# Kernel tuning notes

Hardware: AMD Instinct MI355X
Metric: run time of the kernel (lower is better)

The kernel has to match this reference:

```python
import jax, jax.numpy as jnp
import numpy as np

NUM_HEADS = 16


def setup_inputs() -> dict:
    key = jax.random.key(0)
    k1, k2, k3, k4 = jax.random.split(key, 4)
    B, S, D = 2, 2048, 1024
    x = jax.random.normal(k1, (B, S, D), dtype=jnp.float32)
    W_qkv = jax.random.normal(k2, (D, 3 * D), dtype=jnp.float32) * (1.0 / np.sqrt(D))
    b_qkv = jax.random.normal(k3, (3 * D,), dtype=jnp.float32) * 0.02
    W_out = jax.random.normal(k4, (D, D), dtype=jnp.float32) * (1.0 / np.sqrt(D))
    return {"x": x, "W_qkv": W_qkv, "b_qkv": b_qkv, "W_out": W_out}


def reference(x, W_qkv, b_qkv, W_out):
    B, S, D = x.shape
    H = NUM_HEADS
    Hd = D // H
    scale = 1.0 / np.sqrt(Hd)

    qkv = x @ W_qkv + b_qkv                      # [B, S, 3D]
    q, k, v = jnp.split(qkv, 3, axis=-1)
    # [B, H, S, Hd]
    q = q.reshape(B, S, H, Hd).transpose(0, 2, 1, 3)
    k = k.reshape(B, S, H, Hd).transpose(0, 2, 1, 3)
    v = v.reshape(B, S, H, Hd).transpose(0, 2, 1, 3)

    scores = jnp.einsum('bhqd,bhkd->bhqk', q, k) * scale  # [B, H, S, S]
    causal = jnp.triu(jnp.full((S, S), -jnp.inf, dtype=scores.dtype), k=1)
    scores = scores + causal
    attn = jax.nn.softmax(scores.astype(jnp.float32), axis=-1).astype(q.dtype)

    ctx = jnp.einsum('bhqk,bhkd->bhqd', attn, v)           # [B, H, S, Hd]
    ctx = ctx.transpose(0, 2, 1, 3).reshape(B, S, D)
    return ctx @ W_out
```

## Files before the change

kernel.cpp:

```cpp
#include <hip/hip_runtime.h>
#include <hip/hip_bf16.h>

typedef __bf16 bf16x8 __attribute__((ext_vector_type(8)));
typedef float f32x4 __attribute__((ext_vector_type(4)));

typedef __attribute__((address_space(1))) void gv_t;
typedef __attribute__((address_space(3))) void lv_t;

__device__ __forceinline__ unsigned short f2bf(float f) {
    unsigned int u = __float_as_uint(f);
    unsigned int r = (u + 0x7fffu + ((u >> 16) & 1u)) >> 16;
    return (unsigned short)r;
}

__device__ __forceinline__ unsigned int cvt_pk_bf16(float a, float b) {
    unsigned int r;
    asm("v_cvt_pk_bf16_f32 %0, %1, %2" : "=v"(r) : "v"(a), "v"(b));
    return r;
}

__global__ __launch_bounds__(1024) void preprocess(const float* __restrict__ x,
                                                   const float* __restrict__ Wqkv,
                                                   const float* __restrict__ Wout,
                                                   unsigned short* __restrict__ x_bf,
                                                   unsigned short* __restrict__ wqkvT,
                                                   unsigned short* __restrict__ woutT) {
    const int bid = blockIdx.x, t = threadIdx.x;
    if (bid < 1024) {
        int i = bid * 1024 + t;
        float4 v = reinterpret_cast<const float4*>(x)[i];
        ushort4 o;
        o.x = f2bf(v.x); o.y = f2bf(v.y); o.z = f2bf(v.z); o.w = f2bf(v.w);
        reinterpret_cast<ushort4*>(x_bf)[i] = o;
        return;
    }
    __shared__ float tile[32][33];
    const int tx = t & 31, ty = t >> 5;
    const float* in;
    unsigned short* out;
    int K, N, n0, k0;
    if (bid < 4096) {
        int e = bid - 1024;
        in = Wqkv; out = wqkvT; K = 1024; N = 3072;
        n0 = (e % 96) * 32; k0 = (e / 96) * 32;
    } else {
        int e = bid - 4096;
        in = Wout; out = woutT; K = 1024; N = 1024;
        n0 = (e % 32) * 32; k0 = (e / 32) * 32;
    }
    tile[ty][tx] = in[(size_t)(k0 + ty) * N + (n0 + tx)];
    __syncthreads();
    out[(size_t)(n0 + ty) * K + (k0 + tx)] = f2bf(tile[tx][ty]);
}

template <bool BIAS, bool OUT_BF16, bool QSCALE>
__global__ __launch_bounds__(256) void gemm_bt(const unsigned short* __restrict__ A,
                                               const unsigned short* __restrict__ Bt,
                                               const float* __restrict__ bias,
                                               void* __restrict__ Cv,
                                               int M, int N, int K) {
    __shared__ alignas(16) unsigned short As[128 * 32];
    __shared__ alignas(16) unsigned short Bs[128 * 32];

    const int t = threadIdx.x;
    const int lane = t & 63;
    const int wid = t >> 6;
    const int wr = wid >> 1, wc = wid & 1;
    const int nwg = gridDim.x * gridDim.y;
    const int lin = blockIdx.y * gridDim.x + blockIdx.x;
    const int cpx = nwg >> 3;
    const int swz = (lin & 7) * cpx + (lin >> 3);
    const int m0 = (swz / gridDim.x) * 128, n0 = (swz % gridDim.x) * 128;

    f32x4 acc[4][4] = {};

    for (int k0 = 0; k0 < K; k0 += 32) {
#pragma unroll
        for (int i = 0; i < 2; ++i) {
            int c = i * 256 + t;
            int row = c >> 2;
            int col = (c & 3) * 8;
            const unsigned short* ga = A + (size_t)(m0 + row) * K + k0 + col;
            const unsigned short* gb = Bt + (size_t)(n0 + row) * K + k0 + col;
            __builtin_amdgcn_global_load_lds((gv_t*)ga, (lv_t*)(As + c * 8), 16, 0, 0);
            __builtin_amdgcn_global_load_lds((gv_t*)gb, (lv_t*)(Bs + c * 8), 16, 0, 0);
        }
        __syncthreads();

        bf16x8 af[4], bfr[4];
#pragma unroll
        for (int i = 0; i < 4; ++i)
            af[i] = *reinterpret_cast<const bf16x8*>(As + (wr * 64 + i * 16 + (lane & 15)) * 32 + (lane >> 4) * 8);
#pragma unroll
        for (int j = 0; j < 4; ++j)
            bfr[j] = *reinterpret_cast<const bf16x8*>(Bs + (wc * 64 + j * 16 + (lane & 15)) * 32 + (lane >> 4) * 8);
#pragma unroll
        for (int i = 0; i < 4; ++i)
#pragma unroll
            for (int j = 0; j < 4; ++j)
                acc[i][j] = __builtin_amdgcn_mfma_f32_16x16x32_bf16(af[i], bfr[j], acc[i][j], 0, 0, 0);
        __syncthreads();
    }

#pragma unroll
    for (int i = 0; i < 4; ++i) {
        int row = m0 + wr * 64 + i * 16 + (lane >> 4) * 4;
#pragma unroll
        for (int j = 0; j < 4; ++j) {
            int col = n0 + wc * 64 + j * 16 + (lane & 15);
            float bv = 0.0f;
            if (BIAS) bv = bias[col];
#pragma unroll
            for (int r = 0; r < 4; ++r) {
                float v = acc[i][j][r] + bv;
                if constexpr (QSCALE) { if (col < 1024) v *= 0.125f; }
                if constexpr (OUT_BF16)
                    ((unsigned short*)Cv)[(size_t)(row + r) * N + col] = f2bf(v);
                else
                    ((float*)Cv)[(size_t)(row + r) * N + col] = v;
            }
        }
    }
}

__global__ __launch_bounds__(512) void attn_fwd(const unsigned short* __restrict__ qkv,
                                                unsigned short* __restrict__ ctx,
                                                int S) {
    const int TD = 3072, D = 1024;
    __shared__ alignas(16) unsigned short Ks[2][128 * 64];
    __shared__ alignas(16) unsigned short Vt[2][128 * 64];
    __shared__ alignas(16) unsigned short Ps[8][16 * 64];

    const int t = threadIdx.x, lane = t & 63;
    const int w_all = t >> 6;
    const int w_loc = w_all & 3;
    const bool is_hi = (w_all < 4);
    const int l15 = lane & 15, l4 = lane >> 4;
    const int lin = blockIdx.y * 16 + blockIdx.x;
    const int swz = (lin & 7) * 64 + (lin >> 3);
    const int pid = swz & 15;
    const int bh = swz >> 4;
    const int b = bh >> 4, h = bh & 15;
    const int QT_lo = pid, QT_hi = 31 - pid;
    const int QT = is_hi ? QT_hi : QT_lo;

    const size_t base = ((size_t)b * S) * TD + (size_t)h * 64;
    const unsigned short* qp = qkv + base;
    const unsigned short* kp = qkv + base + D;
    const unsigned short* vp = qkv + base + 2 * D;

    bf16x8 aq[2];
    {
        const unsigned short* g = qp + (size_t)(QT * 64 + w_loc * 16 + l15) * TD + l4 * 8;
        aq[0] = *reinterpret_cast<const bf16x8*>(g);
        aq[1] = *reinterpret_cast<const bf16x8*>(g + 32);
    }

    f32x4 oc[4] = {};
    float lR = 0.f;
    const float L2E = 1.44269504f;
    const float MFIX = 12.0f * L2E;

    auto stageK2 = [&](int j0, int buf) {
        int j1 = min(j0 + 1, QT_hi);
#pragma unroll
        for (int rnd = 0; rnd < 2; ++rnd) {
            int c = rnd * 512 + t;
            int row = c >> 3, hh = c & 7;
            int gkv = (row < 64) ? (j0 * 64 + row) : (j1 * 64 + (row & 63));
            const unsigned short* src = kp + (size_t)gkv * TD + ((hh ^ (row & 7)) * 8);
            __builtin_amdgcn_global_load_lds((gv_t*)src, (lv_t*)(Ks[buf] + c * 8), 16, 0, 0);
        }
    };
    const int v_hd = (t & 31) * 2, v_kvb = (t >> 5) * 8;
    unsigned int vv[8];
    auto loadV2 = [&](int j0) {
        int j1 = min(j0 + 1, QT_hi);
        int gkv = (v_kvb < 64) ? (j0 * 64 + v_kvb) : (j1 * 64 + (v_kvb & 63));
        const unsigned short* vsrc = vp + (size_t)gkv * TD + v_hd;
#pragma unroll
        for (int e = 0; e < 8; ++e)
            vv[e] = *reinterpret_cast<const unsigned int*>(vsrc + (size_t)e * TD);
    };
    auto writeV2 = [&](int buf) {
        unsigned int r0[4], r1[4];
#pragma unroll
        for (int i = 0; i < 4; ++i) {
            r0[i] = __builtin_amdgcn_perm(vv[2 * i + 1], vv[2 * i], 0x05040100u);
            r1[i] = __builtin_amdgcn_perm(vv[2 * i + 1], vv[2 * i], 0x07060302u);
        }
        int half = v_kvb >> 6;
        int kv0 = v_kvb & 63;
        int g0 = (kv0 >> 3) ^ (v_hd & 7);
        int g1 = (kv0 >> 3) ^ ((v_hd + 1) & 7);
        unsigned short* vb = Vt[buf] + half * 4096;
        *reinterpret_cast<uint4*>(vb + v_hd * 64 + g0 * 8) = make_uint4(r0[0], r0[1], r0[2], r0[3]);
        *reinterpret_cast<uint4*>(vb + (v_hd + 1) * 64 + g1 * 8) = make_uint4(r1[0], r1[1], r1[2], r1[3]);
    };

    auto compute = [&](bool diag, int buf, int half) {
        const unsigned short* Kb = Ks[buf] + half * 4096;
        const unsigned short* Vb = Vt[buf] + half * 4096;
        f32x4 sc[4];
        __builtin_amdgcn_s_setprio(1);
#pragma unroll
        for (int jn = 0; jn < 4; ++jn) {
            f32x4 s = {};
#pragma unroll
            for (int kk = 0; kk < 2; ++kk) {
                int row = jn * 16 + l15;
                int g = (kk * 4 + l4) ^ (l15 & 7);
                bf16x8 ak = *reinterpret_cast<const bf16x8*>(Kb + row * 64 + g * 8);
                s = __builtin_amdgcn_mfma_f32_16x16x32_bf16(ak, aq[kk], s, 0, 0, 0);
            }
            sc[jn] = s;
        }
        __builtin_amdgcn_s_setprio(0);
        if (diag) {
            int ql = w_loc * 16 + l15;
#pragma unroll
            for (int jn = 0; jn < 4; ++jn)
#pragma unroll
                for (int r = 0; r < 4; ++r)
                    if (jn * 16 + l4 * 4 + r > ql) sc[jn][r] = -1e30f;
        }
        float ps = 0.f;
#pragma unroll
        for (int jn = 0; jn < 4; ++jn) {
            float p0 = exp2f(sc[jn][0] * L2E - MFIX);
            float p1 = exp2f(sc[jn][1] * L2E - MFIX);
            float p2 = exp2f(sc[jn][2] * L2E - MFIX);
            float p3 = exp2f(sc[jn][3] * L2E - MFIX);
            sc[jn][0] = p0; sc[jn][1] = p1; sc[jn][2] = p2; sc[jn][3] = p3;
            ps += (p0 + p1) + (p2 + p3);
        }
        lR += ps;
        const int q = l15;
#pragma unroll
        for (int jn = 0; jn < 4; ++jn) {
            unsigned int lo = cvt_pk_bf16(sc[jn][0], sc[jn][1]);
            unsigned int hi = cvt_pk_bf16(sc[jn][2], sc[jn][3]);
            int kv0 = jn * 16 + l4 * 4;
            int g = (kv0 >> 3) ^ (q & 7);
            *reinterpret_cast<uint2*>(Ps[w_all] + q * 64 + g * 8 + (kv0 & 7)) = make_uint2(lo, hi);
        }
        __builtin_amdgcn_s_setprio(1);
#pragma unroll
        for (int kk = 0; kk < 2; ++kk) {
            int gq = (kk * 4 + l4) ^ (q & 7);
            bf16x8 bp = *reinterpret_cast<const bf16x8*>(Ps[w_all] + q * 64 + gq * 8);
#pragma unroll
            for (int jc = 0; jc < 4; ++jc) {
                int hdrow = jc * 16 + l15;
                int gv = (kk * 4 + l4) ^ (l15 & 7);
                bf16x8 av = *reinterpret_cast<const bf16x8*>(Vb + hdrow * 64 + gv * 8);
                oc[jc] = __builtin_amdgcn_mfma_f32_16x16x32_bf16(av, bp, oc[jc], 0, 0, 0);
            }
        }
        __builtin_amdgcn_s_setprio(0);
    };

    stageK2(0, 0);
    loadV2(0);
    writeV2(0);
    __syncthreads();

    for (int jj = 0; jj <= QT_hi; jj += 2) {
        const int cur = (jj >> 1) & 1, nxt = cur ^ 1;
        const bool have_next = (jj + 2 <= QT_hi);
        if (have_next) {
            stageK2(jj + 2, nxt);
            loadV2(jj + 2);
        }
        if (jj <= QT) compute(jj == QT, cur, 0);
        if (jj + 1 <= QT) compute(jj + 1 == QT, cur, 1);
        if (have_next) writeV2(nxt);
        __syncthreads();
    }

    {
        lR += __shfl_xor(lR, 16);
        lR += __shfl_xor(lR, 32);
        float inv = 1.0f / lR;
        size_t qg = (size_t)QT * 64 + w_loc * 16 + l15;
        unsigned short* crow = ctx + ((size_t)b * S + qg) * D + h * 64;
#pragma unroll
        for (int jc = 0; jc < 4; ++jc) {
            unsigned int pk0 = cvt_pk_bf16(oc[jc][0] * inv, oc[jc][1] * inv);
            unsigned int pk1 = cvt_pk_bf16(oc[jc][2] * inv, oc[jc][3] * inv);
            *reinterpret_cast<uint2*>(crow + jc * 16 + l4 * 4) = make_uint2(pk0, pk1);
        }
    }
}

extern "C" void kernel_launch(void* const* d_in, const int* in_sizes, int n_in,
                              void* d_out, int out_size, void* d_ws, size_t ws_size,
                              hipStream_t stream) {
    const float* x = (const float*)d_in[0];
    const float* Wqkv = (const float*)d_in[1];
    const float* bqkv = (const float*)d_in[2];
    const float* Wout = (const float*)d_in[3];
    float* out = (float*)d_out;

    const int B = 2, S = 2048, D = 1024, TD = 3072;
    const int M = B * S;

    char* ws = (char*)d_ws;
    unsigned short* x_bf  = (unsigned short*)(ws);
    unsigned short* wqkvT = (unsigned short*)(ws + 8388608);
    unsigned short* woutT = (unsigned short*)(ws + 14680064);
    unsigned short* qkv   = (unsigned short*)(ws + 16777216);
    unsigned short* ctx   = (unsigned short*)(ws + 41943040);

    preprocess<<<dim3(5120), dim3(1024), 0, stream>>>(x, Wqkv, Wout, x_bf, wqkvT, woutT);

    gemm_bt<true, true, true><<<dim3(TD / 128, M / 128), dim3(256), 0, stream>>>(
        x_bf, wqkvT, bqkv, (void*)qkv, M, TD, D);

    attn_fwd<<<dim3(16, 32), dim3(512), 0, stream>>>(qkv, ctx, S);

    gemm_bt<false, false, false><<<dim3(D / 128, M / 128), dim3(256), 0, stream>>>(
        ctx, woutT, nullptr, (void*)out, M, D, D);
}
```

Measured before the change: 122.1 us.

## Split paired causal attention tiles into interleaved KV tasks across wave groups

The two query tiles a block processes (lo and hi) now form one combined stream of 33 KV-tile tasks. Each of the two wave groups takes alternate tasks and keeps partial output and row sums for both tiles. The partials are then reduced through shared memory before normalisation. The aim is to balance work between the wave groups, which were previously idle for very different numbers of iterations, at the cost of doubled accumulator registers and an extra LDS reduction step.

```diff
diff --git a/kernel.cpp b/kernel.cpp
--- a/kernel.cpp
+++ b/kernel.cpp
@@ -133,8 +133,8 @@
 
     const int t = threadIdx.x, lane = t & 63;
     const int w_all = t >> 6;
+    const int g = w_all >> 2;
     const int w_loc = w_all & 3;
-    const bool is_hi = (w_all < 4);
     const int l15 = lane & 15, l4 = lane >> 4;
     const int lin = blockIdx.y * 16 + blockIdx.x;
     const int swz = (lin & 7) * 64 + (lin >> 3);
@@ -142,41 +142,48 @@
     const int bh = swz >> 4;
     const int b = bh >> 4, h = bh & 15;
     const int QT_lo = pid, QT_hi = 31 - pid;
-    const int QT = is_hi ? QT_hi : QT_lo;
+    const int nHi = QT_hi + 1;
 
     const size_t base = ((size_t)b * S) * TD + (size_t)h * 64;
     const unsigned short* qp = qkv + base;
     const unsigned short* kp = qkv + base + D;
     const unsigned short* vp = qkv + base + 2 * D;
 
-    bf16x8 aq[2];
+    bf16x8 aq2[2][2];
     {
-        const unsigned short* g = qp + (size_t)(QT * 64 + w_loc * 16 + l15) * TD + l4 * 8;
-        aq[0] = *reinterpret_cast<const bf16x8*>(g);
-        aq[1] = *reinterpret_cast<const bf16x8*>(g + 32);
-    }
-
-    f32x4 oc[4] = {};
-    float lR = 0.f;
+        const unsigned short* gh = qp + (size_t)(QT_hi * 64 + w_loc * 16 + l15) * TD + l4 * 8;
+        aq2[0][0] = *reinterpret_cast<const bf16x8*>(gh);
+        aq2[0][1] = *reinterpret_cast<const bf16x8*>(gh + 32);
+        const unsigned short* gl = qp + (size_t)(QT_lo * 64 + w_loc * 16 + l15) * TD + l4 * 8;
+        aq2[1][0] = *reinterpret_cast<const bf16x8*>(gl);
+        aq2[1][1] = *reinterpret_cast<const bf16x8*>(gl + 32);
+    }
+
+    f32x4 oc2[2][4] = {};
+    float lR2[2] = {0.f, 0.f};
     const float L2E = 1.44269504f;
     const float MFIX = 12.0f * L2E;
 
-    auto stageK2 = [&](int j0, int buf) {
-        int j1 = min(j0 + 1, QT_hi);
+    auto stageK2 = [&](int p, int buf) {
 #pragma unroll
         for (int rnd = 0; rnd < 2; ++rnd) {
             int c = rnd * 512 + t;
             int row = c >> 3, hh = c & 7;
-            int gkv = (row < 64) ? (j0 * 64 + row) : (j1 * 64 + (row & 63));
+            int task = 2 * p + (row >> 6);
+            if (task > 32) task = 32;
+            int j = (task < nHi) ? task : task - nHi;
+            int gkv = j * 64 + (row & 63);
             const unsigned short* src = kp + (size_t)gkv * TD + ((hh ^ (row & 7)) * 8);
             __builtin_amdgcn_global_load_lds((gv_t*)src, (lv_t*)(Ks[buf] + c * 8), 16, 0, 0);
         }
     };
     const int v_hd = (t & 31) * 2, v_kvb = (t >> 5) * 8;
     unsigned int vv[8];
-    auto loadV2 = [&](int j0) {
-        int j1 = min(j0 + 1, QT_hi);
-        int gkv = (v_kvb < 64) ? (j0 * 64 + v_kvb) : (j1 * 64 + (v_kvb & 63));
+    auto loadV2 = [&](int p) {
+        int task = 2 * p + (v_kvb >> 6);
+        if (task > 32) task = 32;
+        int j = (task < nHi) ? task : task - nHi;
+        int gkv = j * 64 + (v_kvb & 63);
         const unsigned short* vsrc = vp + (size_t)gkv * TD + v_hd;
 #pragma unroll
         for (int e = 0; e < 8; ++e)
@@ -189,18 +196,22 @@
             r0[i] = __builtin_amdgcn_perm(vv[2 * i + 1], vv[2 * i], 0x05040100u);
             r1[i] = __builtin_amdgcn_perm(vv[2 * i + 1], vv[2 * i], 0x07060302u);
         }
-        int half = v_kvb >> 6;
+        int slot = v_kvb >> 6;
         int kv0 = v_kvb & 63;
         int g0 = (kv0 >> 3) ^ (v_hd & 7);
         int g1 = (kv0 >> 3) ^ ((v_hd + 1) & 7);
-        unsigned short* vb = Vt[buf] + half * 4096;
+        unsigned short* vb = Vt[buf] + slot * 4096;
         *reinterpret_cast<uint4*>(vb + v_hd * 64 + g0 * 8) = make_uint4(r0[0], r0[1], r0[2], r0[3]);
         *reinterpret_cast<uint4*>(vb + (v_hd + 1) * 64 + g1 * 8) = make_uint4(r1[0], r1[1], r1[2], r1[3]);
     };
 
-    auto compute = [&](bool diag, int buf, int half) {
-        const unsigned short* Kb = Ks[buf] + half * 4096;
-        const unsigned short* Vb = Vt[buf] + half * 4096;
+    auto compute = [&](int task, int buf, int slot) {
+        const int tile = (task < nHi) ? 0 : 1;
+        const int j = (task < nHi) ? task : task - nHi;
+        const bool diag = (j == ((tile == 0) ? QT_hi : QT_lo));
+        const unsigned short* Kb = Ks[buf] + slot * 4096;
+        const unsigned short* Vb = Vt[buf] + slot * 4096;
+        const bf16x8* aq = aq2[tile];
         f32x4 sc[4];
         __builtin_amdgcn_s_setprio(1);
 #pragma unroll
@@ -209,8 +220,8 @@
 #pragma unroll
             for (int kk = 0; kk < 2; ++kk) {
                 int row = jn * 16 + l15;
-                int g = (kk * 4 + l4) ^ (l15 & 7);
-                bf16x8 ak = *reinterpret_cast<const bf16x8*>(Kb + row * 64 + g * 8);
+                int gk = (kk * 4 + l4) ^ (l15 & 7);
+                bf16x8 ak = *reinterpret_cast<const bf16x8*>(Kb + row * 64 + gk * 8);
                 s = __builtin_amdgcn_mfma_f32_16x16x32_bf16(ak, aq[kk], s, 0, 0, 0);
             }
             sc[jn] = s;
@@ -234,15 +245,15 @@
             sc[jn][0] = p0; sc[jn][1] = p1; sc[jn][2] = p2; sc[jn][3] = p3;
             ps += (p0 + p1) + (p2 + p3);
         }
-        lR += ps;
+        lR2[tile] += ps;
         const int q = l15;
 #pragma unroll
         for (int jn = 0; jn < 4; ++jn) {
             unsigned int lo = cvt_pk_bf16(sc[jn][0], sc[jn][1]);
             unsigned int hi = cvt_pk_bf16(sc[jn][2], sc[jn][3]);
             int kv0 = jn * 16 + l4 * 4;
-            int g = (kv0 >> 3) ^ (q & 7);
-            *reinterpret_cast<uint2*>(Ps[w_all] + q * 64 + g * 8 + (kv0 & 7)) = make_uint2(lo, hi);
+            int gg = (kv0 >> 3) ^ (q & 7);
+            *reinterpret_cast<uint2*>(Ps[w_all] + q * 64 + gg * 8 + (kv0 & 7)) = make_uint2(lo, hi);
         }
         __builtin_amdgcn_s_setprio(1);
 #pragma unroll
@@ -254,7 +265,7 @@
                 int hdrow = jc * 16 + l15;
                 int gv = (kk * 4 + l4) ^ (l15 & 7);
                 bf16x8 av = *reinterpret_cast<const bf16x8*>(Vb + hdrow * 64 + gv * 8);
-                oc[jc] = __builtin_amdgcn_mfma_f32_16x16x32_bf16(av, bp, oc[jc], 0, 0, 0);
+                oc2[tile][jc] = __builtin_amdgcn_mfma_f32_16x16x32_bf16(av, bp, oc2[tile][jc], 0, 0, 0);
             }
         }
         __builtin_amdgcn_s_setprio(0);
@@ -265,20 +276,40 @@
     writeV2(0);
     __syncthreads();
 
-    for (int jj = 0; jj <= QT_hi; jj += 2) {
-        const int cur = (jj >> 1) & 1, nxt = cur ^ 1;
-        const bool have_next = (jj + 2 <= QT_hi);
+    for (int p = 0; p <= 16; ++p) {
+        const int cur = p & 1, nxt = cur ^ 1;
+        const bool have_next = (p < 16);
         if (have_next) {
-            stageK2(jj + 2, nxt);
-            loadV2(jj + 2);
-        }
-        if (jj <= QT) compute(jj == QT, cur, 0);
-        if (jj + 1 <= QT) compute(jj + 1 == QT, cur, 1);
+            stageK2(p + 1, nxt);
+            loadV2(p + 1);
+        }
+        int task = 2 * p + g;
+        if (task <= 32) compute(task, cur, g);
         if (have_next) writeV2(nxt);
         __syncthreads();
     }
 
-    {
+    float* X = reinterpret_cast<float*>(&Ks[0][0]);
+    float* Y = reinterpret_cast<float*>(&Vt[0][0]);
+    const int idx = (w_loc * 64 + lane) * 17;
+    if (g == 1) {
+#pragma unroll
+        for (int jc = 0; jc < 4; ++jc)
+#pragma unroll
+            for (int r = 0; r < 4; ++r)
+                X[idx + jc * 4 + r] = oc2[0][jc][r];
+        X[idx + 16] = lR2[0];
+    } else {
+#pragma unroll
+        for (int jc = 0; jc < 4; ++jc)
+#pragma unroll
+            for (int r = 0; r < 4; ++r)
+                Y[idx + jc * 4 + r] = oc2[1][jc][r];
+        Y[idx + 16] = lR2[1];
+    }
+    __syncthreads();
+
+    auto epi = [&](f32x4* oc, float lR, int QT) {
         lR += __shfl_xor(lR, 16);
         lR += __shfl_xor(lR, 32);
         float inv = 1.0f / lR;
@@ -290,6 +321,22 @@
             unsigned int pk1 = cvt_pk_bf16(oc[jc][2] * inv, oc[jc][3] * inv);
             *reinterpret_cast<uint2*>(crow + jc * 16 + l4 * 4) = make_uint2(pk0, pk1);
         }
+    };
+
+    if (g == 0) {
+#pragma unroll
+        for (int jc = 0; jc < 4; ++jc)
+#pragma unroll
+            for (int r = 0; r < 4; ++r)
+                oc2[0][jc][r] += X[idx + jc * 4 + r];
+        epi(oc2[0], lR2[0] + X[idx + 16], QT_hi);
+    } else {
+#pragma unroll
+        for (int jc = 0; jc < 4; ++jc)
+#pragma unroll
+            for (int r = 0; r < 4; ++r)
+                oc2[1][jc][r] += Y[idx + jc * 4 + r];
+        epi(oc2[1], lR2[1] + Y[idx + 16], QT_lo);
     }
 }
 
```

After: 128.8 us. 5.5% more time.
